# Kernel tuning notes

Measured on AMD Instinct MI355X. Metric: run time of the kernel, lower is better.

Reference implementation:

```python
import jax, jax.numpy as jnp
import numpy as np

N, L, H, M, D = 4096, 4096, 8, 64, 64

def setup_inputs() -> dict:
    key = jax.random.key(0)
    kq, kk, kv = jax.random.split(key, 3)
    queries = jax.random.normal(kq, (N, H, M), dtype=jnp.float32)
    keys = jax.random.normal(kk, (L, H, M), dtype=jnp.float32)
    values = jax.random.normal(kv, (L, H, D), dtype=jnp.float32)
    return {"queries": queries, "keys": keys, "values": values}

def reference(queries, keys, values):
    # scores: [n, l, h] = sigmoid(q . k) per head
    attention_num = jax.nn.sigmoid(jnp.einsum('nhm,lhm->nlh', queries, keys))
    # normalizer: sum over l -> [n, h] (torch code broadcasts via wasteful repeat)
    attention_normalizer = jnp.sum(attention_num, axis=1, keepdims=True)  # [n,1,h]
    attention = attention_num / attention_normalizer  # [n,l,h]
    # dropout p=0.0 -> identity
    attn_output = jnp.einsum('nlh,lhd->nhd', attention, values)
    return attn_output
```

## Files before the change

### kernel.cpp

```cpp
#include <hip/hip_runtime.h>
#include <stdint.h>


typedef __bf16 bf16x8 __attribute__((ext_vector_type(8)));
typedef __bf16 bf16x2 __attribute__((ext_vector_type(2)));
typedef float  f32x2  __attribute__((ext_vector_type(2)));
typedef float  f32x16 __attribute__((ext_vector_type(16)));
typedef unsigned u32x4 __attribute__((ext_vector_type(4)));

constexpr int NH = 8, MD = 64, NL = 4096, NN = 4096;
constexpr size_t ONUM_ELEMS = (size_t)NN * NH * MD;
constexpr size_t Z_ELEMS    = (size_t)NN * NH;
constexpr size_t KB_ELEMS   = (size_t)NH * NL * MD;
constexpr size_t VTB_ELEMS  = (size_t)NH * NL * MD;

__device__ __forceinline__ unsigned packbf2(float a, float b) {
  bf16x2 t = __builtin_convertvector((f32x2){a, b}, bf16x2);
  return __builtin_bit_cast(unsigned, t);
}

__device__ __forceinline__ void glds16(const void* g, void* l) {
  __builtin_amdgcn_global_load_lds(
      (const __attribute__((address_space(1))) unsigned int*)g,
      (__attribute__((address_space(3))) unsigned int*)l, 16, 0, 0);
}

__global__ __launch_bounds__(256) void diffattn_prepass(
    const float* __restrict__ Kg, const float* __restrict__ Vg,
    unsigned short* __restrict__ Kb, unsigned short* __restrict__ Vtb) {
  __shared__ __attribute__((aligned(16))) unsigned short Vt_lds[64 * 64];
  const int tid = threadIdx.x;
  const int h = blockIdx.x & 7;
  const int t = blockIdx.x >> 3;

#pragma unroll
  for (int e = 0; e < 2; ++e) {
    const int g = tid * 2 + e;
    const int l = g >> 3, c = g & 7;
    const float* kp = Kg + (((size_t)(t * 64 + l) * NH + h) * MD) + c * 8;
    const float4 a = *(const float4*)kp;
    const float4 b = *(const float4*)(kp + 4);
    unsigned out[4] = {packbf2(a.x, a.y), packbf2(a.z, a.w),
                       packbf2(b.x, b.y), packbf2(b.z, b.w)};
    unsigned short* dst =
        Kb + ((size_t)h * NL + t * 64 + l) * MD + ((c ^ (l & 7)) * 8);
    *(uint4*)dst = *(const uint4*)out;
  }

  {
    const int lr = tid & 63, dbase = (tid >> 6) * 16;
    const int pl = (lr & 0x33) | ((lr & 4) << 1) | ((lr & 8) >> 1);
    const float* vp = Vg + (((size_t)(t * 64 + lr) * NH + h) * MD) + dbase;
#pragma unroll
    for (int i = 0; i < 4; ++i) {
      const float4 v = *(const float4*)(vp + i * 4);
      const int d0 = dbase + i * 4;
      Vt_lds[(d0 + 0) * 64 + pl] = __builtin_bit_cast(unsigned short, (__bf16)v.x);
      Vt_lds[(d0 + 1) * 64 + pl] = __builtin_bit_cast(unsigned short, (__bf16)v.y);
      Vt_lds[(d0 + 2) * 64 + pl] = __builtin_bit_cast(unsigned short, (__bf16)v.z);
      Vt_lds[(d0 + 3) * 64 + pl] = __builtin_bit_cast(unsigned short, (__bf16)v.w);
    }
  }
  __syncthreads();
#pragma unroll
  for (int e = 0; e < 2; ++e) {
    const int g = tid * 2 + e;
    const int d = g >> 3, cl = g & 7;
    const uint4 chunk = *(const uint4*)&Vt_lds[d * 64 + cl * 8];
    unsigned short* dst = Vtb + ((size_t)(h * 64 + t) * 64 + d) * 64 +
                          ((cl ^ (d & 7)) * 8);
    *(uint4*)dst = chunk;
  }
}

__global__ __launch_bounds__(256, 4) void diffattn_partial(
    const float* __restrict__ Qg, const unsigned short* __restrict__ Kb,
    const unsigned short* __restrict__ Vtb, unsigned short* __restrict__ Onum,
    float* __restrict__ Zp, int nsplit, int lLen) {
  __shared__ __attribute__((aligned(16))) unsigned short Ksh[2][64 * 64];
  __shared__ __attribute__((aligned(16))) unsigned short Vtsh[2][64 * 64];

  const int tid  = threadIdx.x;
  const int w    = tid >> 6;
  const int lane = tid & 63;
  const int col  = lane & 31;
  const int hi   = lane >> 5;

  const int h     = blockIdx.x & 7;
  const int tmp   = blockIdx.x >> 3;
  const int split = tmp % nsplit;
  const int n0    = (tmp / nsplit) * 128;
  const int lBeg  = split * lLen;

  bf16x8 qf[4];
  {
    const float* qp = Qg + ((size_t)(n0 + w * 32 + col) * NH + h) * MD;
    const float c = -1.4426950408889634f;
#pragma unroll
    for (int kc = 0; kc < 4; ++kc) {
      const float4 x = *(const float4*)(qp + kc * 16 + hi * 8);
      const float4 y = *(const float4*)(qp + kc * 16 + hi * 8 + 4);
      bf16x8 f;
      f[0] = (__bf16)(c * x.x); f[1] = (__bf16)(c * x.y);
      f[2] = (__bf16)(c * x.z); f[3] = (__bf16)(c * x.w);
      f[4] = (__bf16)(c * y.x); f[5] = (__bf16)(c * y.y);
      f[6] = (__bf16)(c * y.z); f[7] = (__bf16)(c * y.w);
      qf[kc] = f;
    }
  }

  f32x16 oacc[2];
#pragma unroll
  for (int i = 0; i < 16; ++i) { oacc[0][i] = 0.f; oacc[1][i] = 0.f; }
  float zacc = 0.f;
  const f32x16 zf = {};

  const char* kgh = (const char*)(Kb + (size_t)h * NL * MD);
  const char* vgh = (const char*)(Vtb + (size_t)h * NL * MD);
  const int o = w * 2048 + lane * 16;
  const int T = lLen >> 6;

  {
    const char* kgb = kgh + (size_t)lBeg * 128;
    const char* vgb = vgh + (size_t)lBeg * 128;
    glds16(kgb + o,        (char*)Ksh[0]  + w * 2048);
    glds16(kgb + o + 1024, (char*)Ksh[0]  + w * 2048 + 1024);
    glds16(vgb + o,        (char*)Vtsh[0] + w * 2048);
    glds16(vgb + o + 1024, (char*)Vtsh[0] + w * 2048 + 1024);
  }

  for (int t = 0; t < T; ++t) {
    const int cur = t & 1;
    __syncthreads();
    if (t + 1 < T) {
      const char* kgb = kgh + (size_t)(lBeg + (t + 1) * 64) * 128;
      const char* vgb = vgh + (size_t)(lBeg + (t + 1) * 64) * 128;
      glds16(kgb + o,        (char*)Ksh[cur ^ 1]  + w * 2048);
      glds16(kgb + o + 1024, (char*)Ksh[cur ^ 1]  + w * 2048 + 1024);
      glds16(vgb + o,        (char*)Vtsh[cur ^ 1] + w * 2048);
      glds16(vgb + o + 1024, (char*)Vtsh[cur ^ 1] + w * 2048 + 1024);
    }

    f32x16 d1[2];
#pragma unroll
    for (int lh = 0; lh < 2; ++lh) {
      const int rowK = lh * 32 + col;
      const char* kp = (const char*)Ksh[cur] + rowK * 128;
      const int swk = rowK & 7;
      {
        const bf16x8 kf = *(const bf16x8*)(kp + ((hi ^ swk) * 16));
        d1[lh] = __builtin_amdgcn_mfma_f32_32x32x16_bf16(kf, qf[0], zf, 0, 0, 0);
      }
#pragma unroll
      for (int kc = 1; kc < 4; ++kc) {
        const bf16x8 kf = *(const bf16x8*)(kp + (((kc << 1) | hi) ^ swk) * 16);
        d1[lh] = __builtin_amdgcn_mfma_f32_32x32x16_bf16(kf, qf[kc], d1[lh], 0, 0, 0);
      }
    }

    const char* vb = (const char*)Vtsh[cur];
    bf16x8 vfA[2][2];
#pragma unroll
    for (int c = 0; c < 2; ++c)
#pragma unroll
      for (int ds = 0; ds < 2; ++ds) {
        const int rowV = ds * 32 + col;
        vfA[c][ds] = *(const bf16x8*)(vb + rowV * 128 +
                                      (((c << 1) | hi) ^ (rowV & 7)) * 16);
      }

    unsigned pk[2][8];
#pragma unroll
    for (int lh = 0; lh < 2; ++lh) {
#pragma unroll
      for (int p = 0; p < 8; ++p) {
        const float eA = __builtin_amdgcn_exp2f(d1[lh][2 * p]);
        const float eB = __builtin_amdgcn_exp2f(d1[lh][2 * p + 1]);
        const float tA = 1.0f + eA;
        const float tB = 1.0f + eB;
        const float r  = __builtin_amdgcn_rcpf(tA * tB);
        const float sa = r * tB;
        const float sb = r * tA;
        zacc += sa + sb;
        pk[lh][p] = packbf2(sa, sb);
      }
    }

#pragma unroll
    for (int c = 0; c < 2; ++c) {
      const bf16x8 pf = __builtin_bit_cast(bf16x8, *(const u32x4*)&pk[0][c * 4]);
#pragma unroll
      for (int ds = 0; ds < 2; ++ds)
        oacc[ds] = __builtin_amdgcn_mfma_f32_32x32x16_bf16(pf, vfA[c][ds],
                                                           oacc[ds], 0, 0, 0);
    }
#pragma unroll
    for (int c = 0; c < 2; ++c)
#pragma unroll
      for (int ds = 0; ds < 2; ++ds) {
        const int rowV = ds * 32 + col;
        vfA[c][ds] = *(const bf16x8*)(vb + rowV * 128 +
                                      ((((c + 2) << 1 | hi)) ^ (rowV & 7)) * 16);
      }
#pragma unroll
    for (int c = 0; c < 2; ++c) {
      const bf16x8 pf = __builtin_bit_cast(bf16x8, *(const u32x4*)&pk[1][c * 4]);
#pragma unroll
      for (int ds = 0; ds < 2; ++ds)
        oacc[ds] = __builtin_amdgcn_mfma_f32_32x32x16_bf16(pf, vfA[c][ds],
                                                           oacc[ds], 0, 0, 0);
    }
  }

  const float zrow = zacc + __shfl_xor(zacc, 32, 64);
  if (hi == 0)
    Zp[(size_t)split * Z_ELEMS + (size_t)(n0 + w * 32 + col) * NH + h] = zrow;

  unsigned short* onum = Onum + (size_t)split * ONUM_ELEMS;
#pragma unroll
  for (int ds = 0; ds < 2; ++ds) {
    const int d = ds * 32 + col;
#pragma unroll
    for (int r = 0; r < 16; ++r) {
      const int row = (r & 3) + 8 * (r >> 2) + 4 * hi;
      onum[((size_t)(n0 + w * 32 + row) * NH + h) * MD + d] =
          __builtin_bit_cast(unsigned short, (__bf16)oacc[ds][r]);
    }
  }
}

__global__ __launch_bounds__(256) void diffattn_combine(
    const unsigned short* __restrict__ Onum, const float* __restrict__ Zp,
    float* __restrict__ Og, int nsplit) {
  const int idx = blockIdx.x * 256 + threadIdx.x;
  if (idx >= (int)(ONUM_ELEMS / 8)) return;
  const int nh = idx >> 3;
  const int c8 = (idx & 7) * 8;
  float z = 0.f;
  float acc[8] = {0.f, 0.f, 0.f, 0.f, 0.f, 0.f, 0.f, 0.f};
  for (int s = 0; s < nsplit; ++s) {
    z += Zp[(size_t)s * Z_ELEMS + nh];
    const uint4 t = *(const uint4*)(Onum + (size_t)s * ONUM_ELEMS +
                                    (size_t)nh * MD + c8);
    const unsigned u[4] = {t.x, t.y, t.z, t.w};
#pragma unroll
    for (int j = 0; j < 4; ++j) {
      acc[2 * j]     += __builtin_bit_cast(float, u[j] << 16);
      acc[2 * j + 1] += __builtin_bit_cast(float, u[j] & 0xffff0000u);
    }
  }
  const float zi = __builtin_amdgcn_rcpf(z);
  float4 r0 = make_float4(acc[0] * zi, acc[1] * zi, acc[2] * zi, acc[3] * zi);
  float4 r1 = make_float4(acc[4] * zi, acc[5] * zi, acc[6] * zi, acc[7] * zi);
  float* out = Og + (size_t)nh * MD + c8;
  *(float4*)out = r0;
  *(float4*)(out + 4) = r1;
}

extern "C" void kernel_launch(void* const* d_in, const int* in_sizes, int n_in,
                              void* d_out, int out_size, void* d_ws, size_t ws_size,
                              hipStream_t stream) {
  const float* Q = (const float*)d_in[0];
  const float* K = (const float*)d_in[1];
  const float* V = (const float*)d_in[2];
  float* O = (float*)d_out;

  const size_t conv_bytes = (KB_ELEMS + VTB_ELEMS) * sizeof(unsigned short);
  int nsplit = 4;
  while (nsplit > 1 &&
         (size_t)nsplit * (ONUM_ELEMS * 2 + Z_ELEMS * 4) + conv_bytes > ws_size)
    nsplit >>= 1;

  unsigned short* Onum = (unsigned short*)d_ws;
  float* Zp = (float*)(Onum + (size_t)nsplit * ONUM_ELEMS);
  unsigned short* Kbb = (unsigned short*)(Zp + (size_t)nsplit * Z_ELEMS);
  unsigned short* Vtb = Kbb + KB_ELEMS;

  const int lLen = NL / nsplit;
  diffattn_prepass<<<dim3(8 * (NL / 64)), dim3(256), 0, stream>>>(K, V, Kbb, Vtb);
  diffattn_partial<<<dim3(8 * 32 * nsplit), dim3(256), 0, stream>>>(
      Q, Kbb, Vtb, Onum, Zp, nsplit, lLen);
  diffattn_combine<<<dim3((ONUM_ELEMS / 8 + 255) / 256), dim3(256), 0, stream>>>(
      Onum, Zp, O, nsplit);
}
```

Before: 128.9 us.

## Software-pipeline QK of the next tile with PV of the previous tile

```diff
diff --git a/kernel.cpp b/kernel.cpp
--- a/kernel.cpp
+++ b/kernel.cpp
@@ -78,7 +78,7 @@
     const unsigned short* __restrict__ Vtb, unsigned short* __restrict__ Onum,
     float* __restrict__ Zp, int nsplit, int lLen) {
   __shared__ __attribute__((aligned(16))) unsigned short Ksh[2][64 * 64];
-  __shared__ __attribute__((aligned(16))) unsigned short Vtsh[2][64 * 64];
+  __shared__ __attribute__((aligned(16))) unsigned short Vtsh[3][64 * 64];
 
   const int tid  = threadIdx.x;
   const int w    = tid >> 6;
@@ -120,96 +120,93 @@
   const int o = w * 2048 + lane * 16;
   const int T = lLen >> 6;
 
-  {
-    const char* kgb = kgh + (size_t)lBeg * 128;
-    const char* vgb = vgh + (size_t)lBeg * 128;
-    glds16(kgb + o,        (char*)Ksh[0]  + w * 2048);
-    glds16(kgb + o + 1024, (char*)Ksh[0]  + w * 2048 + 1024);
-    glds16(vgb + o,        (char*)Vtsh[0] + w * 2048);
-    glds16(vgb + o + 1024, (char*)Vtsh[0] + w * 2048 + 1024);
-  }
-
-  for (int t = 0; t < T; ++t) {
-    const int cur = t & 1;
+  auto prefetch = [&](int tile, int kb, int vb) {
+    const char* kgb = kgh + (size_t)(lBeg + tile * 64) * 128;
+    const char* vgb = vgh + (size_t)(lBeg + tile * 64) * 128;
+    glds16(kgb + o,        (char*)Ksh[kb] + w * 2048);
+    glds16(kgb + o + 1024, (char*)Ksh[kb] + w * 2048 + 1024);
+    glds16(vgb + o,        (char*)Vtsh[vb] + w * 2048);
+    glds16(vgb + o + 1024, (char*)Vtsh[vb] + w * 2048 + 1024);
+  };
+  auto qk_lh = [&](const char* kb, int lh) -> f32x16 {
+    const int rowK = lh * 32 + col;
+    const char* kp = kb + rowK * 128;
+    const int swk = rowK & 7;
+    const bf16x8 kf0 = *(const bf16x8*)(kp + ((hi ^ swk) * 16));
+    f32x16 d = __builtin_amdgcn_mfma_f32_32x32x16_bf16(kf0, qf[0], zf, 0, 0, 0);
+#pragma unroll
+    for (int kc = 1; kc < 4; ++kc) {
+      const bf16x8 kf = *(const bf16x8*)(kp + (((kc << 1) | hi) ^ swk) * 16);
+      d = __builtin_amdgcn_mfma_f32_32x32x16_bf16(kf, qf[kc], d, 0, 0, 0);
+    }
+    return d;
+  };
+  auto sig8 = [&](const f32x16& d, unsigned* pkout) {
+    float s[16];
+#pragma unroll
+    for (int r = 0; r < 16; ++r) {
+      const float e = __builtin_amdgcn_exp2f(d[r]);
+      s[r] = __builtin_amdgcn_rcpf(1.0f + e);
+      zacc += s[r];
+    }
+#pragma unroll
+    for (int p = 0; p < 8; ++p) pkout[p] = packbf2(s[2 * p], s[2 * p + 1]);
+  };
+  auto pv_chunk = [&](const char* vb, int kc2, const unsigned* pk4) {
+    const bf16x8 pf = __builtin_bit_cast(bf16x8, *(const u32x4*)pk4);
+#pragma unroll
+    for (int ds = 0; ds < 2; ++ds) {
+      const int rowV = ds * 32 + col;
+      const bf16x8 vfr = *(const bf16x8*)(vb + rowV * 128 +
+                                          (((kc2 << 1) | hi) ^ (rowV & 7)) * 16);
+      oacc[ds] = __builtin_amdgcn_mfma_f32_32x32x16_bf16(pf, vfr, oacc[ds], 0, 0, 0);
+    }
+  };
+
+  unsigned pkA[16], pkB[16];
+  int iPrev = 0, iNext = 2;
+
+  prefetch(0, 0, 0);
+  __syncthreads();
+  if (T > 1) prefetch(1, 1, 1);
+  {
+    const char* kb = (const char*)Ksh[0];
+    f32x16 da = qk_lh(kb, 0);
+    sig8(da, &pkA[0]);
+    f32x16 db = qk_lh(kb, 1);
+    sig8(db, &pkA[8]);
+  }
+
+  auto step = [&](int t, const unsigned* pp, unsigned* pc) {
     __syncthreads();
-    if (t + 1 < T) {
-      const char* kgb = kgh + (size_t)(lBeg + (t + 1) * 64) * 128;
-      const char* vgb = vgh + (size_t)(lBeg + (t + 1) * 64) * 128;
-      glds16(kgb + o,        (char*)Ksh[cur ^ 1]  + w * 2048);
-      glds16(kgb + o + 1024, (char*)Ksh[cur ^ 1]  + w * 2048 + 1024);
-      glds16(vgb + o,        (char*)Vtsh[cur ^ 1] + w * 2048);
-      glds16(vgb + o + 1024, (char*)Vtsh[cur ^ 1] + w * 2048 + 1024);
-    }
-
-    f32x16 d1[2];
-#pragma unroll
-    for (int lh = 0; lh < 2; ++lh) {
-      const int rowK = lh * 32 + col;
-      const char* kp = (const char*)Ksh[cur] + rowK * 128;
-      const int swk = rowK & 7;
-      {
-        const bf16x8 kf = *(const bf16x8*)(kp + ((hi ^ swk) * 16));
-        d1[lh] = __builtin_amdgcn_mfma_f32_32x32x16_bf16(kf, qf[0], zf, 0, 0, 0);
-      }
-#pragma unroll
-      for (int kc = 1; kc < 4; ++kc) {
-        const bf16x8 kf = *(const bf16x8*)(kp + (((kc << 1) | hi) ^ swk) * 16);
-        d1[lh] = __builtin_amdgcn_mfma_f32_32x32x16_bf16(kf, qf[kc], d1[lh], 0, 0, 0);
-      }
-    }
-
-    const char* vb = (const char*)Vtsh[cur];
-    bf16x8 vfA[2][2];
-#pragma unroll
-    for (int c = 0; c < 2; ++c)
-#pragma unroll
-      for (int ds = 0; ds < 2; ++ds) {
-        const int rowV = ds * 32 + col;
-        vfA[c][ds] = *(const bf16x8*)(vb + rowV * 128 +
-                                      (((c << 1) | hi) ^ (rowV & 7)) * 16);
-      }
-
-    unsigned pk[2][8];
-#pragma unroll
-    for (int lh = 0; lh < 2; ++lh) {
-#pragma unroll
-      for (int p = 0; p < 8; ++p) {
-        const float eA = __builtin_amdgcn_exp2f(d1[lh][2 * p]);
-        const float eB = __builtin_amdgcn_exp2f(d1[lh][2 * p + 1]);
-        const float tA = 1.0f + eA;
-        const float tB = 1.0f + eB;
-        const float r  = __builtin_amdgcn_rcpf(tA * tB);
-        const float sa = r * tB;
-        const float sb = r * tA;
-        zacc += sa + sb;
-        pk[lh][p] = packbf2(sa, sb);
-      }
-    }
-
-#pragma unroll
-    for (int c = 0; c < 2; ++c) {
-      const bf16x8 pf = __builtin_bit_cast(bf16x8, *(const u32x4*)&pk[0][c * 4]);
-#pragma unroll
-      for (int ds = 0; ds < 2; ++ds)
-        oacc[ds] = __builtin_amdgcn_mfma_f32_32x32x16_bf16(pf, vfA[c][ds],
-                                                           oacc[ds], 0, 0, 0);
-    }
-#pragma unroll
-    for (int c = 0; c < 2; ++c)
-#pragma unroll
-      for (int ds = 0; ds < 2; ++ds) {
-        const int rowV = ds * 32 + col;
-        vfA[c][ds] = *(const bf16x8*)(vb + rowV * 128 +
-                                      ((((c + 2) << 1 | hi)) ^ (rowV & 7)) * 16);
-      }
-#pragma unroll
-    for (int c = 0; c < 2; ++c) {
-      const bf16x8 pf = __builtin_bit_cast(bf16x8, *(const u32x4*)&pk[1][c * 4]);
-#pragma unroll
-      for (int ds = 0; ds < 2; ++ds)
-        oacc[ds] = __builtin_amdgcn_mfma_f32_32x32x16_bf16(pf, vfA[c][ds],
-                                                           oacc[ds], 0, 0, 0);
-    }
+    if (t + 1 < T) prefetch(t + 1, (t + 1) & 1, iNext);
+    const char* kb  = (const char*)Ksh[t & 1];
+    const char* vbP = (const char*)Vtsh[iPrev];
+    f32x16 da = qk_lh(kb, 0);
+    pv_chunk(vbP, 0, pp + 0);
+    pv_chunk(vbP, 1, pp + 4);
+    sig8(da, pc);
+    f32x16 db = qk_lh(kb, 1);
+    pv_chunk(vbP, 2, pp + 8);
+    pv_chunk(vbP, 3, pp + 12);
+    sig8(db, pc + 8);
+    iPrev = (iPrev == 2) ? 0 : iPrev + 1;
+    iNext = (iNext == 2) ? 0 : iNext + 1;
+  };
+
+  int t = 1;
+  while (t < T) {
+    step(t, pkA, pkB); ++t;
+    if (t < T) { step(t, pkB, pkA); ++t; }
+  }
+
+  {
+    const char* vbP = (const char*)Vtsh[iPrev];
+    const unsigned* pp = ((T - 1) & 1) ? pkB : pkA;
+    pv_chunk(vbP, 0, pp + 0);
+    pv_chunk(vbP, 1, pp + 4);
+    pv_chunk(vbP, 2, pp + 8);
+    pv_chunk(vbP, 3, pp + 12);
   }
 
   const float zrow = zacc + __shfl_xor(zacc, 32, 64);
```

New measurement: 123.5 us. 1.04x faster.

## Restructure partial kernel to single-wave blocks covering 64 queries and 32-key tiles

Applied to the files above, without the earlier changes.

```diff
diff --git a/kernel.cpp b/kernel.cpp
--- a/kernel.cpp
+++ b/kernel.cpp
@@ -65,36 +65,37 @@
 #pragma unroll
   for (int e = 0; e < 2; ++e) {
     const int g = tid * 2 + e;
-    const int d = g >> 3, cl = g & 7;
-    const uint4 chunk = *(const uint4*)&Vt_lds[d * 64 + cl * 8];
-    unsigned short* dst = Vtb + ((size_t)(h * 64 + t) * 64 + d) * 64 +
-                          ((cl ^ (d & 7)) * 8);
+    const int d = g >> 3, hf = (g >> 2) & 1, c = g & 3;
+    const uint4 chunk = *(const uint4*)&Vt_lds[d * 64 + hf * 32 + c * 8];
+    unsigned short* dst = Vtb +
+        (((size_t)(h * 128 + t * 2 + hf) * 64 + d) * 32) + ((c ^ (d & 3)) * 8);
     *(uint4*)dst = chunk;
   }
 }
 
-__global__ __launch_bounds__(256, 4) void diffattn_partial(
+__global__ __launch_bounds__(64, 3) void diffattn_partial(
     const float* __restrict__ Qg, const unsigned short* __restrict__ Kb,
     const unsigned short* __restrict__ Vtb, unsigned short* __restrict__ Onum,
     float* __restrict__ Zp, int nsplit, int lLen) {
-  __shared__ __attribute__((aligned(16))) unsigned short Ksh[2][64 * 64];
-  __shared__ __attribute__((aligned(16))) unsigned short Vtsh[2][64 * 64];
-
-  const int tid  = threadIdx.x;
-  const int w    = tid >> 6;
-  const int lane = tid & 63;
+  __shared__ __attribute__((aligned(16))) unsigned short Ksh[32 * 64];
+  __shared__ __attribute__((aligned(16))) unsigned short Vsh[64 * 32];
+
+  const int lane = threadIdx.x;
   const int col  = lane & 31;
   const int hi   = lane >> 5;
 
   const int h     = blockIdx.x & 7;
-  const int tmp   = blockIdx.x >> 3;
-  const int split = tmp % nsplit;
-  const int n0    = (tmp / nsplit) * 128;
+  const int r     = blockIdx.x >> 3;
+  const int split = r % nsplit;
+  const int qt    = r / nsplit;
+  const int n0    = qt * 64;
   const int lBeg  = split * lLen;
-
-  bf16x8 qf[4];
-  {
-    const float* qp = Qg + ((size_t)(n0 + w * 32 + col) * NH + h) * MD;
+  const int T     = lLen >> 5;
+
+  bf16x8 qf[2][4];
+#pragma unroll
+  for (int half = 0; half < 2; ++half) {
+    const float* qp = Qg + ((size_t)(n0 + half * 32 + col) * NH + h) * MD;
     const float c = -1.4426950408889634f;
 #pragma unroll
     for (int kc = 0; kc < 4; ++kc) {
@@ -105,128 +106,107 @@
       f[2] = (__bf16)(c * x.z); f[3] = (__bf16)(c * x.w);
       f[4] = (__bf16)(c * y.x); f[5] = (__bf16)(c * y.y);
       f[6] = (__bf16)(c * y.z); f[7] = (__bf16)(c * y.w);
-      qf[kc] = f;
-    }
-  }
-
-  f32x16 oacc[2];
-#pragma unroll
-  for (int i = 0; i < 16; ++i) { oacc[0][i] = 0.f; oacc[1][i] = 0.f; }
-  float zacc = 0.f;
-  const f32x16 zf = {};
-
-  const char* kgh = (const char*)(Kb + (size_t)h * NL * MD);
-  const char* vgh = (const char*)(Vtb + (size_t)h * NL * MD);
-  const int o = w * 2048 + lane * 16;
-  const int T = lLen >> 6;
-
-  {
-    const char* kgb = kgh + (size_t)lBeg * 128;
-    const char* vgb = vgh + (size_t)lBeg * 128;
-    glds16(kgb + o,        (char*)Ksh[0]  + w * 2048);
-    glds16(kgb + o + 1024, (char*)Ksh[0]  + w * 2048 + 1024);
-    glds16(vgb + o,        (char*)Vtsh[0] + w * 2048);
-    glds16(vgb + o + 1024, (char*)Vtsh[0] + w * 2048 + 1024);
-  }
+      qf[half][kc] = f;
+    }
+  }
+
+  f32x16 oacc[2][2];
+#pragma unroll
+  for (int a = 0; a < 2; ++a)
+#pragma unroll
+    for (int b = 0; b < 2; ++b)
+#pragma unroll
+      for (int i = 0; i < 16; ++i) oacc[a][b][i] = 0.f;
+  float zacc[2] = {0.f, 0.f};
+  const f32x16 zfc = {};
+
+  const char* kg = (const char*)Kb + (size_t)h * NL * MD * 2 + (size_t)lBeg * 128;
+  const char* vg = (const char*)Vtb + (size_t)h * NL * MD * 2 +
+                   ((size_t)(lBeg >> 5)) * 4096;
+
+  auto prefetch = [&](int t) {
+    const char* ks = kg + (size_t)t * 4096;
+    const char* vs = vg + (size_t)t * 4096;
+#pragma unroll
+    for (int i = 0; i < 4; ++i)
+      glds16(ks + i * 1024 + lane * 16, (char*)Ksh + i * 1024);
+#pragma unroll
+    for (int i = 0; i < 4; ++i)
+      glds16(vs + i * 1024 + lane * 16, (char*)Vsh + i * 1024);
+  };
+
+  prefetch(0);
 
   for (int t = 0; t < T; ++t) {
-    const int cur = t & 1;
-    __syncthreads();
-    if (t + 1 < T) {
-      const char* kgb = kgh + (size_t)(lBeg + (t + 1) * 64) * 128;
-      const char* vgb = vgh + (size_t)(lBeg + (t + 1) * 64) * 128;
-      glds16(kgb + o,        (char*)Ksh[cur ^ 1]  + w * 2048);
-      glds16(kgb + o + 1024, (char*)Ksh[cur ^ 1]  + w * 2048 + 1024);
-      glds16(vgb + o,        (char*)Vtsh[cur ^ 1] + w * 2048);
-      glds16(vgb + o + 1024, (char*)Vtsh[cur ^ 1] + w * 2048 + 1024);
-    }
-
-    f32x16 d1[2];
-#pragma unroll
-    for (int lh = 0; lh < 2; ++lh) {
-      const int rowK = lh * 32 + col;
-      const char* kp = (const char*)Ksh[cur] + rowK * 128;
-      const int swk = rowK & 7;
-      {
-        const bf16x8 kf = *(const bf16x8*)(kp + ((hi ^ swk) * 16));
-        d1[lh] = __builtin_amdgcn_mfma_f32_32x32x16_bf16(kf, qf[0], zf, 0, 0, 0);
-      }
-#pragma unroll
-      for (int kc = 1; kc < 4; ++kc) {
-        const bf16x8 kf = *(const bf16x8*)(kp + (((kc << 1) | hi) ^ swk) * 16);
-        d1[lh] = __builtin_amdgcn_mfma_f32_32x32x16_bf16(kf, qf[kc], d1[lh], 0, 0, 0);
-      }
-    }
-
-    const char* vb = (const char*)Vtsh[cur];
-    bf16x8 vfA[2][2];
+    __asm__ volatile("s_waitcnt vmcnt(0)" ::: "memory");
+
+    const int swk = col & 7;
+    bf16x8 kf[4];
+#pragma unroll
+    for (int kc = 0; kc < 4; ++kc)
+      kf[kc] = *(const bf16x8*)((const char*)Ksh + col * 128 +
+                                ((((kc << 1) | hi) ^ swk) * 16));
+    bf16x8 vf[2][2];
 #pragma unroll
     for (int c = 0; c < 2; ++c)
 #pragma unroll
       for (int ds = 0; ds < 2; ++ds) {
-        const int rowV = ds * 32 + col;
-        vfA[c][ds] = *(const bf16x8*)(vb + rowV * 128 +
-                                      (((c << 1) | hi) ^ (rowV & 7)) * 16);
-      }
-
-    unsigned pk[2][8];
-#pragma unroll
-    for (int lh = 0; lh < 2; ++lh) {
+        const int d = ds * 32 + col;
+        vf[c][ds] = *(const bf16x8*)((const char*)Vsh + d * 64 +
+                                     ((((c << 1) | hi) ^ (d & 3)) * 16));
+      }
+    __asm__ volatile("s_waitcnt lgkmcnt(0)" ::: "memory");
+    if (t + 1 < T) prefetch(t + 1);
+
+#pragma unroll
+    for (int half = 0; half < 2; ++half) {
+      f32x16 d1 = __builtin_amdgcn_mfma_f32_32x32x16_bf16(kf[0], qf[half][0],
+                                                          zfc, 0, 0, 0);
+#pragma unroll
+      for (int kc = 1; kc < 4; ++kc)
+        d1 = __builtin_amdgcn_mfma_f32_32x32x16_bf16(kf[kc], qf[half][kc],
+                                                     d1, 0, 0, 0);
+      unsigned pk[8];
 #pragma unroll
       for (int p = 0; p < 8; ++p) {
-        const float eA = __builtin_amdgcn_exp2f(d1[lh][2 * p]);
-        const float eB = __builtin_amdgcn_exp2f(d1[lh][2 * p + 1]);
-        const float tA = 1.0f + eA;
-        const float tB = 1.0f + eB;
-        const float r  = __builtin_amdgcn_rcpf(tA * tB);
-        const float sa = r * tB;
-        const float sb = r * tA;
-        zacc += sa + sb;
-        pk[lh][p] = packbf2(sa, sb);
-      }
-    }
-
-#pragma unroll
-    for (int c = 0; c < 2; ++c) {
-      const bf16x8 pf = __builtin_bit_cast(bf16x8, *(const u32x4*)&pk[0][c * 4]);
-#pragma unroll
-      for (int ds = 0; ds < 2; ++ds)
-        oacc[ds] = __builtin_amdgcn_mfma_f32_32x32x16_bf16(pf, vfA[c][ds],
-                                                           oacc[ds], 0, 0, 0);
-    }
-#pragma unroll
-    for (int c = 0; c < 2; ++c)
-#pragma unroll
-      for (int ds = 0; ds < 2; ++ds) {
-        const int rowV = ds * 32 + col;
-        vfA[c][ds] = *(const bf16x8*)(vb + rowV * 128 +
-                                      ((((c + 2) << 1 | hi)) ^ (rowV & 7)) * 16);
-      }
-#pragma unroll
-    for (int c = 0; c < 2; ++c) {
-      const bf16x8 pf = __builtin_bit_cast(bf16x8, *(const u32x4*)&pk[1][c * 4]);
-#pragma unroll
-      for (int ds = 0; ds < 2; ++ds)
-        oacc[ds] = __builtin_amdgcn_mfma_f32_32x32x16_bf16(pf, vfA[c][ds],
-                                                           oacc[ds], 0, 0, 0);
-    }
-  }
-
-  const float zrow = zacc + __shfl_xor(zacc, 32, 64);
-  if (hi == 0)
-    Zp[(size_t)split * Z_ELEMS + (size_t)(n0 + w * 32 + col) * NH + h] = zrow;
-
+        const float eA = __builtin_amdgcn_exp2f(d1[2 * p]);
+        const float eB = __builtin_amdgcn_exp2f(d1[2 * p + 1]);
+        const float sa = __builtin_amdgcn_rcpf(1.0f + eA);
+        const float sb = __builtin_amdgcn_rcpf(1.0f + eB);
+        zacc[half] += sa + sb;
+        pk[p] = packbf2(sa, sb);
+      }
+#pragma unroll
+      for (int c = 0; c < 2; ++c) {
+        const bf16x8 pf = __builtin_bit_cast(bf16x8, *(const u32x4*)&pk[c * 4]);
+#pragma unroll
+        for (int ds = 0; ds < 2; ++ds)
+          oacc[half][ds] = __builtin_amdgcn_mfma_f32_32x32x16_bf16(
+              pf, vf[c][ds], oacc[half][ds], 0, 0, 0);
+      }
+    }
+  }
+
+#pragma unroll
+  for (int half = 0; half < 2; ++half) {
+    const float zrow = zacc[half] + __shfl_xor(zacc[half], 32, 64);
+    if (hi == 0)
+      Zp[(size_t)split * Z_ELEMS +
+         (size_t)(n0 + half * 32 + col) * NH + h] = zrow;
+  }
   unsigned short* onum = Onum + (size_t)split * ONUM_ELEMS;
 #pragma unroll
-  for (int ds = 0; ds < 2; ++ds) {
-    const int d = ds * 32 + col;
-#pragma unroll
-    for (int r = 0; r < 16; ++r) {
-      const int row = (r & 3) + 8 * (r >> 2) + 4 * hi;
-      onum[((size_t)(n0 + w * 32 + row) * NH + h) * MD + d] =
-          __builtin_bit_cast(unsigned short, (__bf16)oacc[ds][r]);
-    }
-  }
+  for (int half = 0; half < 2; ++half)
+#pragma unroll
+    for (int ds = 0; ds < 2; ++ds) {
+      const int d = ds * 32 + col;
+#pragma unroll
+      for (int r2 = 0; r2 < 16; ++r2) {
+        const int row = (r2 & 3) + 8 * (r2 >> 2) + 4 * hi;
+        onum[((size_t)(n0 + half * 32 + row) * NH + h) * MD + d] =
+            __builtin_bit_cast(unsigned short, (__bf16)oacc[half][ds][r2]);
+      }
+    }
 }
 
 __global__ __launch_bounds__(256) void diffattn_combine(
@@ -266,7 +246,7 @@
   float* O = (float*)d_out;
 
   const size_t conv_bytes = (KB_ELEMS + VTB_ELEMS) * sizeof(unsigned short);
-  int nsplit = 4;
+  int nsplit = 8;
   while (nsplit > 1 &&
          (size_t)nsplit * (ONUM_ELEMS * 2 + Z_ELEMS * 4) + conv_bytes > ws_size)
     nsplit >>= 1;
@@ -278,7 +258,7 @@
 
   const int lLen = NL / nsplit;
   diffattn_prepass<<<dim3(8 * (NL / 64)), dim3(256), 0, stream>>>(K, V, Kbb, Vtb);
-  diffattn_partial<<<dim3(8 * 32 * nsplit), dim3(256), 0, stream>>>(
+  diffattn_partial<<<dim3(8 * (NN / 64) * nsplit), dim3(64), 0, stream>>>(
       Q, Kbb, Vtb, Onum, Zp, nsplit, lLen);
   diffattn_combine<<<dim3((ONUM_ELEMS / 8 + 255) / 256), dim3(256), 0, stream>>>(
       Onum, Zp, O, nsplit);
```

After: 135.8 us. 5.4% more time.
